# Optimization experiments

Hardware: AMD Instinct MI355X
Metric: run time of the kernel (lower is better)

The kernel has to match this reference:

```python
import jax, jax.numpy as jnp
import numpy as np

TEMPERATURE = 8.0  # sqrt(head_dim=64)
NEG_BIG = -10000.0


def setup_inputs() -> dict:
    key = jax.random.key(0)
    kq, kk, kv, km = jax.random.split(key, 4)
    B, H, S, D, K = 4, 8, 1024, 64, 4
    q = jax.random.normal(kq, (B, H, S, D), dtype=jnp.float32)
    k = jax.random.normal(kk, (B, H, S, D), dtype=jnp.float32)
    v = jax.random.normal(kv, (B, H, S, D), dtype=jnp.float32)
    # K binary attention masks, broadcastable to [B,H,S,S]
    mask = jax.random.randint(km, (K, 1, 1, S, S), 0, 2).astype(jnp.float32)
    return {"q": q, "k": k, "v": v, "mask": mask}


def reference(q, k, v, mask):
    # attn: [B,H,S,S]
    attn = jnp.einsum("bhsd,bhtd->bhst", q / TEMPERATURE, k)
    # additive mask: [K,1,1,S,S]
    ext_mask = (1.0 - mask) * NEG_BIG
    # batched over K instead of the original python loop: [K,B,H,S,S]
    probs = jax.nn.softmax(attn[None] + ext_mask, axis=-1)
    # dropout is identity in eval mode (deterministic reference)
    output = jnp.einsum("kbhst,bhtd->kbhsd", probs, v)
    return (output, attn)
```

## Files before the change

kernel.cpp:

```cpp
#include <hip/hip_runtime.h>
#include <hip/hip_bf16.h>
#include <stdint.h>

typedef float f4 __attribute__((ext_vector_type(4)));
typedef short bf8 __attribute__((ext_vector_type(8)));
typedef uint32_t u4 __attribute__((ext_vector_type(4)));
typedef uint32_t u2 __attribute__((ext_vector_type(2)));

#define SDIM 1024
#define DDIM 64
#define NBH  32
#define KM   4
#define NT   16

#define MB_BLK 16384
#define KB_BLK 1024
#define VT_BLK 512

__device__ __forceinline__ unsigned short f2bf(float f) {
  uint32_t u = __builtin_bit_cast(uint32_t, f);
  u += 0x7fffu + ((u >> 16) & 1u);
  return (unsigned short)(u >> 16);
}

#define GLOAD16(gsrc, ldst)                                                  \
  __builtin_amdgcn_global_load_lds(                                          \
      (const __attribute__((address_space(1))) unsigned int*)(gsrc),         \
      (__attribute__((address_space(3))) unsigned int*)(ldst), 16, 0, 0)

__device__ __forceinline__ bf8 lds_ld(const unsigned short* base, int row, int e0) {
  return *(const bf8*)((const char*)base + (((row * 64 + e0) * 2) ^ ((row & 7) << 4)));
}

__global__ __launch_bounds__(256) void prepass(
    const float* __restrict__ k, const float* __restrict__ v,
    const float* __restrict__ mask, unsigned short* __restrict__ kb,
    unsigned short* __restrict__ vt, uint32_t* __restrict__ mb2) {
  __shared__ float tv[64][65];
  const int b = blockIdx.x;
  const int t = threadIdx.x;
  if (b < MB_BLK) {
    int gid = b * 256 + t;
    float mv = mask[gid];
    unsigned long long bal = __ballot(mv > 0.5f);
    int lane = t & 63;
    int m = gid >> 20;
    int r = (gid >> 10) & 1023;
    int c = gid & 1023;
    if (lane == 0)       mb2[m * 32768 + (c >> 5) * 1024 + r] = (uint32_t)bal;
    else if (lane == 32) mb2[m * 32768 + (c >> 5) * 1024 + r] = (uint32_t)(bal >> 32);
  } else if (b < MB_BLK + KB_BLK) {
    int base = ((b - MB_BLK) * 256 + t) * 8;
    f4 a = *(const f4*)(k + base);
    f4 c = *(const f4*)(k + base + 4);
    bf8 o;
    o[0] = (short)f2bf(a[0]); o[1] = (short)f2bf(a[1]);
    o[2] = (short)f2bf(a[2]); o[3] = (short)f2bf(a[3]);
    o[4] = (short)f2bf(c[0]); o[5] = (short)f2bf(c[1]);
    o[6] = (short)f2bf(c[2]); o[7] = (short)f2bf(c[3]);
    *(bf8*)(kb + base) = o;
  } else {
    int vb = b - MB_BLK - KB_BLK;
    int bh = vb >> 4;
    int s0 = (vb & 15) * 64;
    int sr = t >> 2, c0 = (t & 3) * 16;
    const float* vp = v + ((size_t)(bh * SDIM) + s0 + sr) * DDIM + c0;
#pragma unroll
    for (int i = 0; i < 4; ++i) {
      f4 x = *(const f4*)(vp + 4 * i);
#pragma unroll
      for (int j = 0; j < 4; ++j) tv[sr][c0 + 4 * i + j] = x[j];
    }
    __syncthreads();
    int d = t >> 2, sc0 = (t & 3) * 16;
    unsigned short tmp[16];
#pragma unroll
    for (int i = 0; i < 16; ++i) tmp[i] = f2bf(tv[sc0 + i][d]);
    unsigned short* op = vt + ((size_t)(bh * DDIM) + d) * SDIM + s0 + sc0;
    bf8 o0, o1;
#pragma unroll
    for (int j = 0; j < 8; ++j) { o0[j] = (short)tmp[j]; o1[j] = (short)tmp[j + 8]; }
    *(bf8*)(op) = o0;
    *(bf8*)(op + 8) = o1;
  }
}

__global__ __launch_bounds__(256, 4) void attn_main(
    const float* __restrict__ qf, const unsigned short* __restrict__ kb,
    const unsigned short* __restrict__ vtg, const uint32_t* __restrict__ mb2,
    float* __restrict__ outO, float* __restrict__ attn) {
  __shared__ __align__(16) unsigned short q_s[32 * 64];
  __shared__ __align__(16) unsigned short k_s[2][64 * 64];
  __shared__ __align__(16) unsigned short v_s[2][64 * 64];
  __shared__ __align__(16) unsigned short e_s[32 * 64];

  const int tid = threadIdx.x;
  const int l   = tid & 63;
  const int w   = tid >> 6;
  const int l16 = l & 15;
  const int lg  = l >> 4;
  const int wh  = w & 1;
  const int wc  = w >> 1;

  int bid = (int)blockIdx.x;
  bid = (bid & 7) * 128 + (bid >> 3);
  const int bh = bid >> 5;
  const int r0 = (bid & 31) * 32;

  const int srow = tid >> 3;
  const int sd   = ((tid & 7) ^ (srow & 7)) << 3;
  const unsigned short* ksrc0 = kb  + ((size_t)(bh * SDIM) + srow) * DDIM + sd;
  const unsigned short* ksrc1 = kb  + ((size_t)(bh * SDIM) + srow + 32) * DDIM + sd;
  const unsigned short* vsrc0 = vtg + ((size_t)(bh * DDIM) + srow) * SDIM + sd;
  const unsigned short* vsrc1 = vtg + ((size_t)(bh * DDIM) + srow + 32) * SDIM + sd;

  GLOAD16(ksrc0, &k_s[0][tid * 8]);
  GLOAD16(ksrc1, &k_s[0][(tid + 256) * 8]);
  GLOAD16(vsrc0, &v_s[0][tid * 8]);
  GLOAD16(vsrc1, &v_s[0][(tid + 256) * 8]);

  {
    int row = tid >> 3, d0 = (tid & 7) * 8;
    const float* qp = qf + ((size_t)(bh * SDIM) + r0 + row) * DDIM + d0;
    f4 a = *(const f4*)qp;
    f4 c = *(const f4*)(qp + 4);
    bf8 o;
    o[0] = (short)f2bf(a[0] * 0.125f); o[1] = (short)f2bf(a[1] * 0.125f);
    o[2] = (short)f2bf(a[2] * 0.125f); o[3] = (short)f2bf(a[3] * 0.125f);
    o[4] = (short)f2bf(c[0] * 0.125f); o[5] = (short)f2bf(c[1] * 0.125f);
    o[6] = (short)f2bf(c[2] * 0.125f); o[7] = (short)f2bf(c[3] * 0.125f);
    *(bf8*)((char*)q_s + (((row * 64 + d0) * 2) ^ ((row & 7) << 4))) = o;
  }

  f4 acc[2][4] = {};
  f4 accl[2]   = {};
  bf8 ones;
#pragma unroll
  for (int b = 0; b < 8; ++b) ones[b] = (short)0x3F80;

  const uint32_t* mbase = mb2 + w * 32768 + r0 + l16;

  __syncthreads();

  for (int ct = 0; ct < NT; ++ct) {
    const int cur = ct & 1;

    uint32_t mdw[2][2];
#pragma unroll
    for (int mt2 = 0; mt2 < 2; ++mt2)
#pragma unroll
      for (int kt = 0; kt < 2; ++kt)
        mdw[mt2][kt] = mbase[(ct * 2 + kt) * 1024 + 16 * mt2];

    {
      const int qr = 16 * wh + l16;
      bf8 bq0 = lds_ld(q_s, qr, lg * 8);
      bf8 bq1 = lds_ld(q_s, qr, lg * 8 + 32);
      f4 s[2];
#pragma unroll
      for (int j = 0; j < 2; ++j) {
        const int kc = 32 * wc + 16 * j + l16;
        bf8 ak0 = lds_ld(k_s[cur], kc, lg * 8);
        bf8 ak1 = lds_ld(k_s[cur], kc, lg * 8 + 32);
        f4 sv = {};
        sv = __builtin_amdgcn_mfma_f32_16x16x32_bf16(ak0, bq0, sv, 0, 0, 0);
        sv = __builtin_amdgcn_mfma_f32_16x16x32_bf16(ak1, bq1, sv, 0, 0, 0);
        s[j] = sv;
      }
      float* arow = attn + ((size_t)(bh * SDIM) + r0 + 16 * wh + l16) * SDIM
                    + ct * 64 + 32 * wc + 4 * lg;
      *(f4*)(arow)      = s[0];
      *(f4*)(arow + 16) = s[1];
      const int erow = 16 * wh + l16;
#pragma unroll
      for (int j = 0; j < 2; ++j) {
        u2 ev;
        ev[0] = (uint32_t)f2bf(__expf(s[j][0])) | ((uint32_t)f2bf(__expf(s[j][1])) << 16);
        ev[1] = (uint32_t)f2bf(__expf(s[j][2])) | ((uint32_t)f2bf(__expf(s[j][3])) << 16);
        int col = 32 * wc + 16 * j + 4 * lg;
        *(u2*)((char*)e_s + (((erow * 64 + col) * 2) ^ ((erow & 7) << 4))) = ev;
      }
    }
    __syncthreads();

    if (ct + 1 < NT) {
      const int nxt = cur ^ 1;
      GLOAD16(ksrc0 + (size_t)(ct + 1) * 4096, &k_s[nxt][tid * 8]);
      GLOAD16(ksrc1 + (size_t)(ct + 1) * 4096, &k_s[nxt][(tid + 256) * 8]);
      GLOAD16(vsrc0 + (size_t)(ct + 1) * 64,   &v_s[nxt][tid * 8]);
      GLOAD16(vsrc1 + (size_t)(ct + 1) * 64,   &v_s[nxt][(tid + 256) * 8]);
    }

    {
      bf8 af[2][2];
#pragma unroll
      for (int mt2 = 0; mt2 < 2; ++mt2) {
        const int row = 16 * mt2 + l16;
#pragma unroll
        for (int kt = 0; kt < 2; ++kt) {
          bf8 e = lds_ld(e_s, row, kt * 32 + lg * 8);
          uint32_t bits = (mdw[mt2][kt] >> (lg * 8)) & 0xffu;
          u4 ew = __builtin_bit_cast(u4, e);
#pragma unroll
          for (int d = 0; d < 4; ++d) {
            uint32_t n2 = (bits >> (2 * d)) & 3u;
            uint32_t sp = (n2 * 0x8001u) & 0x00010001u;
            ew[d] &= (sp << 16) - sp;
          }
          af[mt2][kt] = __builtin_bit_cast(bf8, ew);
        }
        accl[mt2] = __builtin_amdgcn_mfma_f32_16x16x32_bf16(af[mt2][0], ones, accl[mt2], 0, 0, 0);
        accl[mt2] = __builtin_amdgcn_mfma_f32_16x16x32_bf16(af[mt2][1], ones, accl[mt2], 0, 0, 0);
      }
#pragma unroll
      for (int nt = 0; nt < 4; ++nt) {
        const int dc = 16 * nt + l16;
        bf8 bv0 = lds_ld(v_s[cur], dc, lg * 8);
        bf8 bv1 = lds_ld(v_s[cur], dc, lg * 8 + 32);
#pragma unroll
        for (int mt2 = 0; mt2 < 2; ++mt2) {
          acc[mt2][nt] = __builtin_amdgcn_mfma_f32_16x16x32_bf16(af[mt2][0], bv0, acc[mt2][nt], 0, 0, 0);
          acc[mt2][nt] = __builtin_amdgcn_mfma_f32_16x16x32_bf16(af[mt2][1], bv1, acc[mt2][nt], 0, 0, 0);
        }
      }
    }
    __syncthreads();
  }

#pragma unroll
  for (int mt2 = 0; mt2 < 2; ++mt2) {
#pragma unroll
    for (int r = 0; r < 4; ++r) {
      float inv = 1.0f / accl[mt2][r];
      int row = 16 * mt2 + 4 * lg + r;
      float* orow = outO + (((size_t)(w * NBH + bh)) * SDIM + r0 + row) * DDIM + l16;
#pragma unroll
      for (int nt = 0; nt < 4; ++nt)
        orow[16 * nt] = acc[mt2][nt][r] * inv;
    }
  }
}

extern "C" void kernel_launch(void* const* d_in, const int* in_sizes, int n_in,
                              void* d_out, int out_size, void* d_ws, size_t ws_size,
                              hipStream_t stream) {
  (void)in_sizes; (void)n_in; (void)out_size; (void)ws_size;
  const float* q    = (const float*)d_in[0];
  const float* k    = (const float*)d_in[1];
  const float* v    = (const float*)d_in[2];
  const float* mask = (const float*)d_in[3];
  float* outO = (float*)d_out;
  float* attn = (float*)d_out + (size_t)KM * NBH * SDIM * DDIM;

  char* ws = (char*)d_ws;
  unsigned short* kb = (unsigned short*)ws;
  unsigned short* vt = (unsigned short*)(ws + (4u << 20));
  uint32_t*       mb = (uint32_t*)(ws + (8u << 20));

  prepass<<<MB_BLK + KB_BLK + VT_BLK, 256, 0, stream>>>(k, v, mask, kb, vt, mb);
  attn_main<<<NBH * 32, 256, 0, stream>>>(q, kb, vt, mb, outO, attn);
}
```

Measured before the change: 57.56 us.

## Unroll tile loop by two with static buffers and earlier prefetch

Unrolls the column-tile loop by two so the double-buffered K/V shared arrays and mask registers use static names instead of indexed buffers. The next tile's K/V global-to-LDS loads now start at the top of each iteration, before the QK MFMAs, and the mask words for the next tile are loaded one iteration ahead. The mid-iteration __syncthreads is replaced by an inline s_waitcnt lgkmcnt(0) plus s_barrier that skips waiting on vector memory. This is meant to hide more load latency, at the cost of more registers, larger code, and reliance on the hand-written barrier being correct with the outstanding async loads.

```diff
diff --git a/kernel.cpp b/kernel.cpp
--- a/kernel.cpp
+++ b/kernel.cpp
@@ -90,8 +90,10 @@
     const unsigned short* __restrict__ vtg, const uint32_t* __restrict__ mb2,
     float* __restrict__ outO, float* __restrict__ attn) {
   __shared__ __align__(16) unsigned short q_s[32 * 64];
-  __shared__ __align__(16) unsigned short k_s[2][64 * 64];
-  __shared__ __align__(16) unsigned short v_s[2][64 * 64];
+  __shared__ __align__(16) unsigned short k_s0[64 * 64];
+  __shared__ __align__(16) unsigned short k_s1[64 * 64];
+  __shared__ __align__(16) unsigned short v_s0[64 * 64];
+  __shared__ __align__(16) unsigned short v_s1[64 * 64];
   __shared__ __align__(16) unsigned short e_s[32 * 64];
 
   const int tid = threadIdx.x;
@@ -114,10 +116,10 @@
   const unsigned short* vsrc0 = vtg + ((size_t)(bh * DDIM) + srow) * SDIM + sd;
   const unsigned short* vsrc1 = vtg + ((size_t)(bh * DDIM) + srow + 32) * SDIM + sd;
 
-  GLOAD16(ksrc0, &k_s[0][tid * 8]);
-  GLOAD16(ksrc1, &k_s[0][(tid + 256) * 8]);
-  GLOAD16(vsrc0, &v_s[0][tid * 8]);
-  GLOAD16(vsrc1, &v_s[0][(tid + 256) * 8]);
+  GLOAD16(ksrc0, k_s0 + tid * 8);
+  GLOAD16(ksrc1, k_s0 + (tid + 256) * 8);
+  GLOAD16(vsrc0, v_s0 + tid * 8);
+  GLOAD16(vsrc1, v_s0 + (tid + 256) * 8);
 
   {
     int row = tid >> 3, d0 = (tid & 7) * 8;
@@ -140,92 +142,93 @@
 
   const uint32_t* mbase = mb2 + w * 32768 + r0 + l16;
 
+  uint32_t mdwA[2][2], mdwB[2][2];
+#pragma unroll
+  for (int mt2 = 0; mt2 < 2; ++mt2)
+#pragma unroll
+    for (int kt = 0; kt < 2; ++kt)
+      mdwA[mt2][kt] = mbase[kt * 1024 + 16 * mt2];
+
   __syncthreads();
 
-  for (int ct = 0; ct < NT; ++ct) {
-    const int cur = ct & 1;
-
-    uint32_t mdw[2][2];
-#pragma unroll
-    for (int mt2 = 0; mt2 < 2; ++mt2)
-#pragma unroll
-      for (int kt = 0; kt < 2; ++kt)
-        mdw[mt2][kt] = mbase[(ct * 2 + kt) * 1024 + 16 * mt2];
-
-    {
-      const int qr = 16 * wh + l16;
-      bf8 bq0 = lds_ld(q_s, qr, lg * 8);
-      bf8 bq1 = lds_ld(q_s, qr, lg * 8 + 32);
-      f4 s[2];
-#pragma unroll
-      for (int j = 0; j < 2; ++j) {
-        const int kc = 32 * wc + 16 * j + l16;
-        bf8 ak0 = lds_ld(k_s[cur], kc, lg * 8);
-        bf8 ak1 = lds_ld(k_s[cur], kc, lg * 8 + 32);
-        f4 sv = {};
-        sv = __builtin_amdgcn_mfma_f32_16x16x32_bf16(ak0, bq0, sv, 0, 0, 0);
-        sv = __builtin_amdgcn_mfma_f32_16x16x32_bf16(ak1, bq1, sv, 0, 0, 0);
-        s[j] = sv;
-      }
-      float* arow = attn + ((size_t)(bh * SDIM) + r0 + 16 * wh + l16) * SDIM
-                    + ct * 64 + 32 * wc + 4 * lg;
-      *(f4*)(arow)      = s[0];
-      *(f4*)(arow + 16) = s[1];
-      const int erow = 16 * wh + l16;
-#pragma unroll
-      for (int j = 0; j < 2; ++j) {
-        u2 ev;
-        ev[0] = (uint32_t)f2bf(__expf(s[j][0])) | ((uint32_t)f2bf(__expf(s[j][1])) << 16);
-        ev[1] = (uint32_t)f2bf(__expf(s[j][2])) | ((uint32_t)f2bf(__expf(s[j][3])) << 16);
-        int col = 32 * wc + 16 * j + 4 * lg;
-        *(u2*)((char*)e_s + (((erow * 64 + col) * 2) ^ ((erow & 7) << 4))) = ev;
-      }
-    }
-    __syncthreads();
-
-    if (ct + 1 < NT) {
-      const int nxt = cur ^ 1;
-      GLOAD16(ksrc0 + (size_t)(ct + 1) * 4096, &k_s[nxt][tid * 8]);
-      GLOAD16(ksrc1 + (size_t)(ct + 1) * 4096, &k_s[nxt][(tid + 256) * 8]);
-      GLOAD16(vsrc0 + (size_t)(ct + 1) * 64,   &v_s[nxt][tid * 8]);
-      GLOAD16(vsrc1 + (size_t)(ct + 1) * 64,   &v_s[nxt][(tid + 256) * 8]);
-    }
-
-    {
-      bf8 af[2][2];
-#pragma unroll
-      for (int mt2 = 0; mt2 < 2; ++mt2) {
-        const int row = 16 * mt2 + l16;
-#pragma unroll
-        for (int kt = 0; kt < 2; ++kt) {
-          bf8 e = lds_ld(e_s, row, kt * 32 + lg * 8);
-          uint32_t bits = (mdw[mt2][kt] >> (lg * 8)) & 0xffu;
-          u4 ew = __builtin_bit_cast(u4, e);
-#pragma unroll
-          for (int d = 0; d < 4; ++d) {
-            uint32_t n2 = (bits >> (2 * d)) & 3u;
-            uint32_t sp = (n2 * 0x8001u) & 0x00010001u;
-            ew[d] &= (sp << 16) - sp;
-          }
-          af[mt2][kt] = __builtin_bit_cast(bf8, ew);
-        }
-        accl[mt2] = __builtin_amdgcn_mfma_f32_16x16x32_bf16(af[mt2][0], ones, accl[mt2], 0, 0, 0);
-        accl[mt2] = __builtin_amdgcn_mfma_f32_16x16x32_bf16(af[mt2][1], ones, accl[mt2], 0, 0, 0);
-      }
-#pragma unroll
-      for (int nt = 0; nt < 4; ++nt) {
-        const int dc = 16 * nt + l16;
-        bf8 bv0 = lds_ld(v_s[cur], dc, lg * 8);
-        bf8 bv1 = lds_ld(v_s[cur], dc, lg * 8 + 32);
-#pragma unroll
-        for (int mt2 = 0; mt2 < 2; ++mt2) {
-          acc[mt2][nt] = __builtin_amdgcn_mfma_f32_16x16x32_bf16(af[mt2][0], bv0, acc[mt2][nt], 0, 0, 0);
-          acc[mt2][nt] = __builtin_amdgcn_mfma_f32_16x16x32_bf16(af[mt2][1], bv1, acc[mt2][nt], 0, 0, 0);
-        }
-      }
-    }
-    __syncthreads();
-  }
+#define BODY(CT, KR, VR, KW, VW, MR, MW, PF)                                   \
+  {                                                                            \
+    if (PF) {                                                                  \
+      GLOAD16(ksrc0 + (size_t)((CT) + 1) * 4096, (KW) + tid * 8);              \
+      GLOAD16(ksrc1 + (size_t)((CT) + 1) * 4096, (KW) + (tid + 256) * 8);      \
+      GLOAD16(vsrc0 + (size_t)((CT) + 1) * 64, (VW) + tid * 8);                \
+      GLOAD16(vsrc1 + (size_t)((CT) + 1) * 64, (VW) + (tid + 256) * 8);        \
+    }                                                                          \
+    {                                                                          \
+      const int qr = 16 * wh + l16;                                            \
+      bf8 bq0 = lds_ld(q_s, qr, lg * 8);                                       \
+      bf8 bq1 = lds_ld(q_s, qr, lg * 8 + 32);                                  \
+      const int kc0 = 32 * wc + l16;                                           \
+      bf8 ak0 = lds_ld((KR), kc0, lg * 8);                                     \
+      bf8 ak1 = lds_ld((KR), kc0, lg * 8 + 32);                                \
+      bf8 ak2 = lds_ld((KR), kc0 + 16, lg * 8);                                \
+      bf8 ak3 = lds_ld((KR), kc0 + 16, lg * 8 + 32);                           \
+      f4 s0 = {}, s1 = {};                                                     \
+      s0 = __builtin_amdgcn_mfma_f32_16x16x32_bf16(ak0, bq0, s0, 0, 0, 0);     \
+      s0 = __builtin_amdgcn_mfma_f32_16x16x32_bf16(ak1, bq1, s0, 0, 0, 0);     \
+      s1 = __builtin_amdgcn_mfma_f32_16x16x32_bf16(ak2, bq0, s1, 0, 0, 0);     \
+      s1 = __builtin_amdgcn_mfma_f32_16x16x32_bf16(ak3, bq1, s1, 0, 0, 0);     \
+      float* arow = attn + ((size_t)(bh * SDIM) + r0 + 16 * wh + l16) * SDIM   \
+                    + (CT) * 64 + 32 * wc + 4 * lg;                            \
+      *(f4*)(arow) = s0;                                                       \
+      *(f4*)(arow + 16) = s1;                                                  \
+      const int erow = 16 * wh + l16;                                          \
+      u2 ev0, ev1;                                                             \
+      ev0[0] = (uint32_t)f2bf(__expf(s0[0])) | ((uint32_t)f2bf(__expf(s0[1])) << 16); \
+      ev0[1] = (uint32_t)f2bf(__expf(s0[2])) | ((uint32_t)f2bf(__expf(s0[3])) << 16); \
+      ev1[0] = (uint32_t)f2bf(__expf(s1[0])) | ((uint32_t)f2bf(__expf(s1[1])) << 16); \
+      ev1[1] = (uint32_t)f2bf(__expf(s1[2])) | ((uint32_t)f2bf(__expf(s1[3])) << 16); \
+      const int colA = 32 * wc + 4 * lg;                                       \
+      *(u2*)((char*)e_s + (((erow * 64 + colA) * 2) ^ ((erow & 7) << 4))) = ev0; \
+      *(u2*)((char*)e_s + (((erow * 64 + colA + 16) * 2) ^ ((erow & 7) << 4))) = ev1; \
+    }                                                                          \
+    asm volatile("s_waitcnt lgkmcnt(0)\n\ts_barrier" ::: "memory");            \
+    {                                                                          \
+      bf8 af[2][2];                                                            \
+      _Pragma("unroll") for (int mt2 = 0; mt2 < 2; ++mt2) {                    \
+        const int row = 16 * mt2 + l16;                                        \
+        _Pragma("unroll") for (int kt = 0; kt < 2; ++kt) {                     \
+          bf8 e = lds_ld(e_s, row, kt * 32 + lg * 8);                          \
+          uint32_t bits = ((MR)[mt2][kt] >> (lg * 8)) & 0xffu;                 \
+          u4 ew = __builtin_bit_cast(u4, e);                                   \
+          _Pragma("unroll") for (int d = 0; d < 4; ++d) {                      \
+            uint32_t n2 = (bits >> (2 * d)) & 3u;                              \
+            uint32_t sp = (n2 * 0x8001u) & 0x00010001u;                        \
+            ew[d] &= (sp << 16) - sp;                                          \
+          }                                                                    \
+          af[mt2][kt] = __builtin_bit_cast(bf8, ew);                           \
+        }                                                                      \
+        accl[mt2] = __builtin_amdgcn_mfma_f32_16x16x32_bf16(af[mt2][0], ones, accl[mt2], 0, 0, 0); \
+        accl[mt2] = __builtin_amdgcn_mfma_f32_16x16x32_bf16(af[mt2][1], ones, accl[mt2], 0, 0, 0); \
+      }                                                                        \
+      _Pragma("unroll") for (int nt = 0; nt < 4; ++nt) {                       \
+        const int dc = 16 * nt + l16;                                          \
+        bf8 bv0 = lds_ld((VR), dc, lg * 8);                                    \
+        bf8 bv1 = lds_ld((VR), dc, lg * 8 + 32);                               \
+        _Pragma("unroll") for (int mt2 = 0; mt2 < 2; ++mt2) {                  \
+          acc[mt2][nt] = __builtin_amdgcn_mfma_f32_16x16x32_bf16(af[mt2][0], bv0, acc[mt2][nt], 0, 0, 0); \
+          acc[mt2][nt] = __builtin_amdgcn_mfma_f32_16x16x32_bf16(af[mt2][1], bv1, acc[mt2][nt], 0, 0, 0); \
+        }                                                                      \
+      }                                                                        \
+    }                                                                          \
+    if (PF) {                                                                  \
+      _Pragma("unroll") for (int mt2 = 0; mt2 < 2; ++mt2)                      \
+        _Pragma("unroll") for (int kt = 0; kt < 2; ++kt)                       \
+          (MW)[mt2][kt] = mbase[(((CT) + 1) * 2 + kt) * 1024 + 16 * mt2];      \
+    }                                                                          \
+    __syncthreads();                                                           \
+  }
+
+  for (int ct2 = 0; ct2 < NT / 2; ++ct2) {
+    BODY(2 * ct2,     k_s0, v_s0, k_s1, v_s1, mdwA, mdwB, true);
+    BODY(2 * ct2 + 1, k_s1, v_s1, k_s0, v_s0, mdwB, mdwA, (ct2 < NT / 2 - 1));
+  }
+#undef BODY
 
 #pragma unroll
   for (int mt2 = 0; mt2 < 2; ++mt2) {
```

Result: faster. 56.02 us (-2.7%).
